# Performance work log

Measured on AMD Instinct MI355X. Metric: run time of the kernel, lower is better.

Reference implementation:

```python
import jax, jax.numpy as jnp
import numpy as np

L, DM, H, DK, DV, DFF = 4, 1024, 16, 64, 64, 4096
B, T, S = 4, 1024, 1024
EPS = 1e-5


def layer_norm(x):
    m = jnp.mean(x, axis=-1, keepdims=True)
    v = jnp.mean((x - m) ** 2, axis=-1, keepdims=True)
    return (x - m) / jnp.sqrt(v + EPS)


def mha(x_q, x_kv, Wq, Wk, Wv, Wo, mask):
    # x_q: [B,Lq,DM], x_kv: [B,Lk,DM], W*: [DM, H*DK] (pre-transposed), Wo: [H*DV, DM]
    b, lq, _ = x_q.shape
    lk = x_kv.shape[1]
    Q = (x_q @ Wq).reshape(b, lq, H, DK).transpose(0, 2, 1, 3)   # [B,H,Lq,DK]
    K = (x_kv @ Wk).reshape(b, lk, H, DK).transpose(0, 2, 1, 3)
    V = (x_kv @ Wv).reshape(b, lk, H, DV).transpose(0, 2, 1, 3)
    scores = jnp.einsum('bhqd,bhkd->bhqk', Q, K) / np.sqrt(DK).astype(np.float32)
    scores = jnp.where(mask[:, None, :, :], jnp.float32(-1e9), scores)  # masked_fill_
    attn = jax.nn.softmax(scores, axis=-1)
    ctx = jnp.einsum('bhqk,bhkv->bqhv', attn, V).reshape(b, lq, H * DV)
    out = ctx @ Wo
    return layer_norm(out + x_q)


def ffn(x, W1, W2):
    return layer_norm(jax.nn.relu(x @ W1) @ W2 + x)


def setup_inputs() -> dict:
    key = jax.random.key(0)
    ks = jax.random.split(key, 12)
    sc = 0.02
    inp = {
        'dec_inputs': jax.random.normal(ks[0], (B, T, DM), jnp.float32),
        'enc_outputs': jax.random.normal(ks[1], (B, S, DM), jnp.float32),
        # causal mask per get_attn_subsequence_mask (True = masked)
        'dec_self_attn_mask': jnp.broadcast_to(jnp.triu(jnp.ones((T, T), bool), k=1), (B, T, T)),
        'dec_enc_attn_mask': jnp.zeros((B, T, S), bool),
        'self_Wq': sc * jax.random.normal(ks[2], (L, DM, H * DK), jnp.float32),
        'self_Wk': sc * jax.random.normal(ks[3], (L, DM, H * DK), jnp.float32),
        'self_Wv': sc * jax.random.normal(ks[4], (L, DM, H * DV), jnp.float32),
        'self_Wo': sc * jax.random.normal(ks[5], (L, H * DV, DM), jnp.float32),
        'cross_Wq': sc * jax.random.normal(ks[6], (L, DM, H * DK), jnp.float32),
        'cross_Wk': sc * jax.random.normal(ks[7], (L, DM, H * DK), jnp.float32),
        'cross_Wv': sc * jax.random.normal(ks[8], (L, DM, H * DV), jnp.float32),
        'cross_Wo': sc * jax.random.normal(ks[9], (L, H * DV, DM), jnp.float32),
        'ffn_W1': sc * jax.random.normal(ks[10], (L, DM, DFF), jnp.float32),
        'ffn_W2': sc * jax.random.normal(ks[11], (L, DFF, DM), jnp.float32),
    }
    return inp


def reference(dec_inputs, enc_outputs, dec_self_attn_mask, dec_enc_attn_mask,
              self_Wq, self_Wk, self_Wv, self_Wo,
              cross_Wq, cross_Wk, cross_Wv, cross_Wo,
              ffn_W1, ffn_W2):
    x = dec_inputs
    for l in range(L):  # fixed small layer count
        x = mha(x, x, self_Wq[l], self_Wk[l], self_Wv[l], self_Wo[l], dec_self_attn_mask)
        x = mha(x, enc_outputs, cross_Wq[l], cross_Wk[l], cross_Wv[l], cross_Wo[l], dec_enc_attn_mask)
        x = ffn(x, ffn_W1[l], ffn_W2[l])
    return x
```

## Files before the change

kernel.cpp:

```cpp
#include <hip/hip_runtime.h>

typedef unsigned short u16;
typedef unsigned int u32;
typedef __bf16 bf16x8 __attribute__((ext_vector_type(8)));
typedef float f32x4 __attribute__((ext_vector_type(4)));

#define TT 1024

__device__ __forceinline__ u16 f2bf(float f) {
  u32 u = __float_as_uint(f);
  u32 r = (u + 0x7fffu + ((u >> 16) & 1u)) >> 16;
  return (u16)r;
}
__device__ __forceinline__ float bf2f(u16 b) {
  return __uint_as_float(((u32)b) << 16);
}

__device__ __forceinline__ void gl_lds16(const void* g, void* l) {
  __builtin_amdgcn_global_load_lds(
      (const __attribute__((address_space(1))) u32*)g,
      (__attribute__((address_space(3))) u32*)l, 16, 0, 0);
}

__global__ __launch_bounds__(256) void k_f32_to_bf16(const float* __restrict__ in,
                                                     u16* __restrict__ out, int n) {
  int i = (blockIdx.x * 256 + threadIdx.x) * 4;
  if (i >= n) return;
  float4 v = *(const float4*)(in + i);
  ushort4 o;
  o.x = f2bf(v.x); o.y = f2bf(v.y); o.z = f2bf(v.z); o.w = f2bf(v.w);
  *(ushort4*)(out + i) = o;
}

__global__ __launch_bounds__(256) void k_init(const float* __restrict__ in,
                                              u16* __restrict__ bfo,
                                              float* __restrict__ fo, int n) {
  int i = (blockIdx.x * 256 + threadIdx.x) * 4;
  if (i >= n) return;
  float4 v = *(const float4*)(in + i);
  ushort4 o;
  o.x = f2bf(v.x); o.y = f2bf(v.y); o.z = f2bf(v.z); o.w = f2bf(v.w);
  *(ushort4*)(bfo + i) = o;
  *(float4*)(fo + i) = v;
}

struct TPack {
  const float* src[8];
  u16* dst[8];
};
__global__ __launch_bounds__(256) void k_transpose(TPack p, int R, int C) {
  __shared__ float tile[32][33];
  const int tx = threadIdx.x & 31;
  const int ty = threadIdx.x >> 5;
  const float* __restrict__ src = p.src[blockIdx.z];
  u16* __restrict__ dst = p.dst[blockIdx.z];
  const int c0 = blockIdx.x * 32;
  const int r0 = blockIdx.y * 32;
#pragma unroll
  for (int i = 0; i < 4; i++)
    tile[ty + i * 8][tx] = src[(size_t)(r0 + ty + i * 8) * C + c0 + tx];
  __syncthreads();
#pragma unroll
  for (int i = 0; i < 4; i++)
    dst[(size_t)(c0 + ty + i * 8) * R + r0 + tx] = f2bf(tile[tx][ty + i * 8]);
}

__global__ __launch_bounds__(256) void k_tbf(const u16* __restrict__ src, int ld,
                                             u16* __restrict__ dst) {
  __shared__ u16 tile[32][33];
  const int r0 = blockIdx.y * 32;
  const int c0 = blockIdx.x * 32;
  const int tr = threadIdx.x >> 3;
  const int tc = (threadIdx.x & 7) * 4;
  ushort4 v = *(const ushort4*)&src[(size_t)(r0 + tr) * ld + c0 + tc];
  tile[tr][tc] = v.x; tile[tr][tc + 1] = v.y; tile[tr][tc + 2] = v.z; tile[tr][tc + 3] = v.w;
  __syncthreads();
  ushort4 o;
  o.x = tile[tc][tr]; o.y = tile[tc + 1][tr]; o.z = tile[tc + 2][tr]; o.w = tile[tc + 3][tr];
  *(ushort4*)&dst[(size_t)(c0 + tr) * 4096 + r0 + tc] = o;
}

template <int OUT_BF16, int RELU, int SPLITK>
__global__ __launch_bounds__(256) void k_gemm_tn(const u16* __restrict__ A,
                                                 const u16* __restrict__ Bt,
                                                 void* __restrict__ Cout,
                                                 void* __restrict__ Cout2,
                                                 int M, int N, int K) {
  __shared__ __attribute__((aligned(16))) u16 sA[128 * 32];
  __shared__ __attribute__((aligned(16))) u16 sB[128 * 32];
  const int tid = threadIdx.x;
  const int wave = tid >> 6;
  const int lane = tid & 63;
  const int quad = lane >> 4;
  const int lc = lane & 15;
  const int m0 = blockIdx.x * 128;
  const int n0 = blockIdx.y * 128;
  const int wr = (wave >> 1) * 64;
  const int wc = (wave & 1) * 64;

  const int Ks = K / SPLITK;
  const size_t kOff = (size_t)blockIdx.z * Ks;

  const int c0 = wave * 2, c1 = wave * 2 + 1;
  const int srow = lane >> 2;
  const int scol = (lane & 3) * 8;

  const u16* a0 = A + (size_t)(m0 + c0 * 16 + srow) * K + kOff + scol;
  const u16* a1 = A + (size_t)(m0 + c1 * 16 + srow) * K + kOff + scol;
  const u16* b0 = Bt + (size_t)(n0 + c0 * 16 + srow) * K + kOff + scol;
  const u16* b1 = Bt + (size_t)(n0 + c1 * 16 + srow) * K + kOff + scol;
  u16* lA0 = sA + c0 * 512;
  u16* lA1 = sA + c1 * 512;
  u16* lB0 = sB + c0 * 512;
  u16* lB1 = sB + c1 * 512;

  f32x4 acc[4][4];
  const f32x4 z4 = {0.f, 0.f, 0.f, 0.f};
#pragma unroll
  for (int i = 0; i < 4; i++)
#pragma unroll
    for (int j = 0; j < 4; j++) acc[i][j] = z4;

  for (int k0 = 0; k0 < Ks; k0 += 32) {
    __syncthreads();
    gl_lds16(a0, lA0);
    gl_lds16(a1, lA1);
    gl_lds16(b0, lB0);
    gl_lds16(b1, lB1);
    a0 += 32; a1 += 32; b0 += 32; b1 += 32;
    __syncthreads();
    bf16x8 af[4], bfr[4];
#pragma unroll
    for (int i = 0; i < 4; i++)
      af[i] = *(const bf16x8*)&sA[(wr + i * 16 + lc) * 32 + quad * 8];
#pragma unroll
    for (int j = 0; j < 4; j++)
      bfr[j] = *(const bf16x8*)&sB[(wc + j * 16 + lc) * 32 + quad * 8];
#pragma unroll
    for (int i = 0; i < 4; i++)
#pragma unroll
      for (int j = 0; j < 4; j++)
        acc[i][j] = __builtin_amdgcn_mfma_f32_16x16x32_bf16(af[i], bfr[j], acc[i][j], 0, 0, 0);
  }

  void* Cw = (SPLITK > 1 && blockIdx.z == 1) ? Cout2 : Cout;
#pragma unroll
  for (int i = 0; i < 4; i++) {
    const int row = m0 + wr + i * 16 + quad * 4;
#pragma unroll
    for (int j = 0; j < 4; j++) {
      const int col = n0 + wc + j * 16 + lc;
#pragma unroll
      for (int r = 0; r < 4; r++) {
        float v = acc[i][j][r];
        if (RELU) v = fmaxf(v, 0.f);
        if (OUT_BF16)
          ((u16*)Cw)[(size_t)(row + r) * N + col] = f2bf(v);
        else
          ((float*)Cw)[(size_t)(row + r) * N + col] = v;
      }
    }
  }
}

template <int CAUSAL>
__global__ __launch_bounds__(256, 4) void k_flash(const u16* __restrict__ Q, int ldq,
                                                  const u16* __restrict__ K, int ldk,
                                                  const u16* __restrict__ Vt,
                                                  u16* __restrict__ O) {
  __shared__ __attribute__((aligned(16))) u16 sK[2][64 * 64];
  __shared__ __attribute__((aligned(16))) u16 sV[2][64 * 64];
  __shared__ __attribute__((aligned(16))) u16 sP[4][16 * 64];
  const int tid = threadIdx.x;
  const int wave = tid >> 6;
  const int lane = tid & 63;
  const int quad = lane >> 4;
  const int lc = lane & 15;
  const int qb = blockIdx.x;
  const int b = blockIdx.y >> 4;
  const int h = blockIdx.y & 15;
  const size_t rowB = (size_t)b * TT;
  const int qrow = qb * 64 + wave * 16;
  const int hc = h * 64;

  const bf16x8 qf0 = *(const bf16x8*)&Q[(rowB + qrow + lc) * ldq + hc + quad * 8];
  const bf16x8 qf1 = *(const bf16x8*)&Q[(rowB + qrow + lc) * ldq + hc + 32 + quad * 8];

  f32x4 o[4];
  float m_r[4], l_r[4];
  const f32x4 z4 = {0.f, 0.f, 0.f, 0.f};
#pragma unroll
  for (int d = 0; d < 4; d++) o[d] = z4;
#pragma unroll
  for (int r = 0; r < 4; r++) { m_r[r] = -1e30f; l_r[r] = 0.f; }

  const float cvt = 1.4426950408889634f / 8.0f;
  u16* myP = sP[wave];
  const int l7 = lc & 7;
  const int swr = (lc >> 2) | ((lc & 1) << 2);
  const int p_lo = wave * 64 + lane;

  const int nkt = CAUSAL ? (qb + 1) : 16;

  auto stage = [&](int cur, int s0) {
#pragma unroll
    for (int half = 0; half < 2; half++) {
      const int p = half * 256 + p_lo;
      const int row = p >> 3;
      const int cb = (p & 7) ^ (row & 7);
      const int p0 = half * 256 + wave * 64;
      gl_lds16(K + (rowB + s0 + row) * (size_t)ldk + hc + cb * 8, &sK[cur][p0 * 8]);
      gl_lds16(Vt + (size_t)(hc + row) * 4096 + rowB + s0 + cb * 8, &sV[cur][p0 * 8]);
    }
  };

  stage(0, 0);
  int cur = 0;
  for (int kt = 0; kt < nkt; kt++) {
    const int s0 = kt * 64;
    __syncthreads();
    if (kt + 1 < nkt) stage(cur ^ 1, s0 + 64);

    f32x4 s[4];
#pragma unroll
    for (int st = 0; st < 4; st++) {
      const int key = st * 16 + lc;
      const bf16x8 kf0 = *(const bf16x8*)&sK[cur][key * 64 + ((quad ^ l7) * 8)];
      const bf16x8 kf1 = *(const bf16x8*)&sK[cur][key * 64 + (((4 + quad) ^ l7) * 8)];
      f32x4 z = z4;
      z = __builtin_amdgcn_mfma_f32_16x16x32_bf16(qf0, kf0, z, 0, 0, 0);
      z = __builtin_amdgcn_mfma_f32_16x16x32_bf16(qf1, kf1, z, 0, 0, 0);
      s[st] = z;
    }

#pragma unroll
    for (int r = 0; r < 4; r++) {
      float sv0 = s[0][r] * cvt, sv1 = s[1][r] * cvt;
      float sv2 = s[2][r] * cvt, sv3 = s[3][r] * cvt;
      if (CAUSAL) {
        const int qg = qrow + quad * 4 + r;
        if (s0 + lc > qg) sv0 = -1e30f;
        if (s0 + 16 + lc > qg) sv1 = -1e30f;
        if (s0 + 32 + lc > qg) sv2 = -1e30f;
        if (s0 + 48 + lc > qg) sv3 = -1e30f;
      }
      float pm = fmaxf(fmaxf(sv0, sv1), fmaxf(sv2, sv3));
      pm = fmaxf(pm, __shfl_xor(pm, 1));
      pm = fmaxf(pm, __shfl_xor(pm, 2));
      pm = fmaxf(pm, __shfl_xor(pm, 4));
      pm = fmaxf(pm, __shfl_xor(pm, 8));
      const float mn = fmaxf(m_r[r], pm);
      const float al = exp2f(m_r[r] - mn);
      m_r[r] = mn;
      const float p0 = exp2f(sv0 - mn);
      const float p1 = exp2f(sv1 - mn);
      const float p2 = exp2f(sv2 - mn);
      const float p3 = exp2f(sv3 - mn);
      l_r[r] = l_r[r] * al + (p0 + p1 + p2 + p3);
      const int row = quad * 4 + r;
      const int sw = quad | ((r & 1) << 2);
      u16* pr = myP + row * 64 + l7;
      pr[(((lc >> 3) | 0) ^ sw) * 8] = f2bf(p0);
      pr[(((lc >> 3) | 2) ^ sw) * 8] = f2bf(p1);
      pr[(((lc >> 3) | 4) ^ sw) * 8] = f2bf(p2);
      pr[(((lc >> 3) | 6) ^ sw) * 8] = f2bf(p3);
#pragma unroll
      for (int d = 0; d < 4; d++) o[d][r] *= al;
    }

#pragma unroll
    for (int c = 0; c < 2; c++) {
      const bf16x8 pf = *(const bf16x8*)&myP[lc * 64 + (((c * 4 + quad) ^ swr) * 8)];
#pragma unroll
      for (int d = 0; d < 4; d++) {
        const int dv = d * 16 + lc;
        const bf16x8 vf = *(const bf16x8*)&sV[cur][dv * 64 + (((c * 4 + quad) ^ l7) * 8)];
        o[d] = __builtin_amdgcn_mfma_f32_16x16x32_bf16(pf, vf, o[d], 0, 0, 0);
      }
    }
    cur ^= 1;
  }

#pragma unroll
  for (int r = 0; r < 4; r++) {
    float l = l_r[r];
    l += __shfl_xor(l, 1);
    l += __shfl_xor(l, 2);
    l += __shfl_xor(l, 4);
    l += __shfl_xor(l, 8);
    const float inv = 1.0f / l;
    const size_t orow = (rowB + qrow + quad * 4 + r) * 1024 + hc;
#pragma unroll
    for (int d = 0; d < 4; d++) O[orow + d * 16 + lc] = f2bf(o[d][r] * inv);
  }
}

template <int NSUM>
__global__ __launch_bounds__(256) void k_ln(const float* __restrict__ y0,
                                            const float* __restrict__ y1,
                                            float* __restrict__ xf,
                                            u16* __restrict__ xb,
                                            float* __restrict__ fout) {
  const int row = blockIdx.x;
  const int tid = threadIdx.x;
  const int lane = tid & 63, wave = tid >> 6;
  const size_t base = (size_t)row * 1024 + tid * 4;
  float4 v = *(const float4*)&y0[base];
  float4 xv = *(const float4*)&xf[base];
  if (NSUM == 2) {
    float4 w = *(const float4*)&y1[base];
    v.x += w.x; v.y += w.y; v.z += w.z; v.w += w.w;
  }
  v.x += xv.x; v.y += xv.y; v.z += xv.z; v.w += xv.w;
  float s = v.x + v.y + v.z + v.w;
  float ss = v.x * v.x + v.y * v.y + v.z * v.z + v.w * v.w;
#pragma unroll
  for (int off = 1; off < 64; off <<= 1) {
    s += __shfl_xor(s, off);
    ss += __shfl_xor(ss, off);
  }
  __shared__ float rs[4], rss[4];
  if (lane == 0) { rs[wave] = s; rss[wave] = ss; }
  __syncthreads();
  const float S = rs[0] + rs[1] + rs[2] + rs[3];
  const float SS = rss[0] + rss[1] + rss[2] + rss[3];
  const float mean = S * (1.f / 1024.f);
  const float var = SS * (1.f / 1024.f) - mean * mean;
  const float inv = rsqrtf(var + 1e-5f);
  const float o0 = (v.x - mean) * inv, o1 = (v.y - mean) * inv;
  const float o2 = (v.z - mean) * inv, o3 = (v.w - mean) * inv;
  float4 fo; fo.x = o0; fo.y = o1; fo.z = o2; fo.w = o3;
  *(float4*)&xf[base] = fo;
  ushort4 ob;
  ob.x = f2bf(o0); ob.y = f2bf(o1); ob.z = f2bf(o2); ob.w = f2bf(o3);
  *(ushort4*)&xb[base] = ob;
  if (fout) *(float4*)&fout[base] = fo;
}

extern "C" void kernel_launch(void* const* d_in, const int* in_sizes, int n_in,
                              void* d_out, int out_size, void* d_ws, size_t ws_size,
                              hipStream_t stream) {
  const float* dec_inputs  = (const float*)d_in[0];
  const float* enc_outputs = (const float*)d_in[1];
  const float* self_Wq = (const float*)d_in[4];
  const float* self_Wk = (const float*)d_in[5];
  const float* self_Wv = (const float*)d_in[6];
  const float* self_Wo = (const float*)d_in[7];
  const float* cross_Wq = (const float*)d_in[8];
  const float* cross_Wk = (const float*)d_in[9];
  const float* cross_Wv = (const float*)d_in[10];
  const float* cross_Wo = (const float*)d_in[11];
  const float* ffn_W1 = (const float*)d_in[12];
  const float* ffn_W2 = (const float*)d_in[13];

  char* ws = (char*)d_ws;
  const size_t MB = 1024 * 1024;
  u16* wq_t = (u16*)(ws + 0 * MB);
  u16* wk_t = (u16*)(ws + 2 * MB);
  u16* wv_t = (u16*)(ws + 4 * MB);
  u16* wo_t = (u16*)(ws + 6 * MB);
  u16* cq_t = (u16*)(ws + 8 * MB);
  u16* ck_t = (u16*)(ws + 10 * MB);
  u16* cv_t = (u16*)(ws + 12 * MB);
  u16* co_t = (u16*)(ws + 14 * MB);
  u16* w1_t = (u16*)(ws + 16 * MB);
  u16* w2_t = (u16*)(ws + 24 * MB);
  u16* encb = (u16*)(ws + 32 * MB);
  u16* xb   = (u16*)(ws + 40 * MB);
  u16* qkv  = (u16*)(ws + 48 * MB);
  u16* kvb  = (u16*)(ws + 56 * MB);
  u16* ctx  = (u16*)(ws + 72 * MB);
  u16* hbuf = (u16*)(ws + 48 * MB);
  float* yb = (float*)(ws + 80 * MB);
  u16* vtb  = (u16*)(ws + 80 * MB);
  float* xf = (float*)(ws + 96 * MB);
  float* ysA = (float*)(ws + 48 * MB);
  float* ysW = (float*)(ws + 0 * MB);

  const int NTOK = 4 * TT * 1024;

  k_init<<<4096, 256, 0, stream>>>(dec_inputs, xb, xf, NTOK);
  k_f32_to_bf16<<<4096, 256, 0, stream>>>(enc_outputs, encb, NTOK);

  for (int l = 0; l < 4; l++) {
    const size_t sqOff = (size_t)l * 1024 * 1024;
    const size_t ffOff = (size_t)l * 4096 * 1024;
    TPack sq;
    sq.src[0] = self_Wq + sqOff;  sq.dst[0] = wq_t;
    sq.src[1] = self_Wk + sqOff;  sq.dst[1] = wk_t;
    sq.src[2] = self_Wv + sqOff;  sq.dst[2] = wv_t;
    sq.src[3] = self_Wo + sqOff;  sq.dst[3] = wo_t;
    sq.src[4] = cross_Wq + sqOff; sq.dst[4] = cq_t;
    sq.src[5] = cross_Wk + sqOff; sq.dst[5] = ck_t;
    sq.src[6] = cross_Wv + sqOff; sq.dst[6] = cv_t;
    sq.src[7] = cross_Wo + sqOff; sq.dst[7] = co_t;
    k_transpose<<<dim3(32, 32, 8), 256, 0, stream>>>(sq, 1024, 1024);
    TPack p1 = sq; p1.src[0] = ffn_W1 + ffOff; p1.dst[0] = w1_t;
    k_transpose<<<dim3(128, 32, 1), 256, 0, stream>>>(p1, 1024, 4096);
    TPack p2 = sq; p2.src[0] = ffn_W2 + ffOff; p2.dst[0] = w2_t;
    k_transpose<<<dim3(32, 128, 1), 256, 0, stream>>>(p2, 4096, 1024);

    k_gemm_tn<1, 0, 1><<<dim3(32, 24), 256, 0, stream>>>(xb, wq_t, qkv, nullptr, 4096, 3072, 1024);
    k_tbf<<<dim3(32, 128), 256, 0, stream>>>(qkv + 2048, 3072, vtb);
    k_flash<1><<<dim3(16, 64), 256, 0, stream>>>(qkv, 3072, qkv + 1024, 3072, vtb, ctx);
    k_gemm_tn<0, 0, 2><<<dim3(32, 8, 2), 256, 0, stream>>>(ctx, wo_t, yb, ysA, 4096, 1024, 1024);
    k_ln<2><<<4096, 256, 0, stream>>>(yb, ysA, xf, xb, nullptr);

    k_gemm_tn<1, 0, 1><<<dim3(32, 8), 256, 0, stream>>>(xb, cq_t, qkv, nullptr, 4096, 1024, 1024);
    k_gemm_tn<1, 0, 1><<<dim3(32, 16), 256, 0, stream>>>(encb, ck_t, kvb, nullptr, 4096, 2048, 1024);
    k_tbf<<<dim3(32, 128), 256, 0, stream>>>(kvb + 1024, 2048, vtb);
    k_flash<0><<<dim3(16, 64), 256, 0, stream>>>(qkv, 1024, kvb, 2048, vtb, ctx);
    k_gemm_tn<0, 0, 2><<<dim3(32, 8, 2), 256, 0, stream>>>(ctx, co_t, yb, ysA, 4096, 1024, 1024);
    k_ln<2><<<4096, 256, 0, stream>>>(yb, ysA, xf, xb, nullptr);

    k_gemm_tn<1, 1, 1><<<dim3(32, 32), 256, 0, stream>>>(xb, w1_t, hbuf, nullptr, 4096, 4096, 1024);
    k_gemm_tn<0, 0, 2><<<dim3(32, 8, 2), 256, 0, stream>>>(hbuf, w2_t, yb, ysW, 4096, 1024, 4096);
    k_ln<2><<<4096, 256, 0, stream>>>(yb, ysW, xf, xb, (l == 3) ? (float*)d_out : nullptr);
  }
}
```

Measured before the change: 1.941 ms.

## Double-buffer GEMM LDS tiles and XOR-swizzle K chunks to avoid bank conflicts

The bf16 MFMA GEMM now keeps two LDS buffers per operand. The next K-tile is prefetched with global_load_lds while the current tile is consumed, which drops one barrier per iteration. It also applies an XOR swizzle to the 8-element K chunk position, on both the global-to-LDS write side and the fragment read side, to reduce LDS bank conflicts. LDS use doubles, which may lower occupancy. Overlap depends on how the compiler places vmcnt waits around the async LDS loads.

```diff
diff --git a/kernel.cpp b/kernel.cpp
--- a/kernel.cpp
+++ b/kernel.cpp
@@ -86,8 +86,8 @@
                                                  void* __restrict__ Cout,
                                                  void* __restrict__ Cout2,
                                                  int M, int N, int K) {
-  __shared__ __attribute__((aligned(16))) u16 sA[128 * 32];
-  __shared__ __attribute__((aligned(16))) u16 sB[128 * 32];
+  __shared__ __attribute__((aligned(16))) u16 sA[2][128 * 32];
+  __shared__ __attribute__((aligned(16))) u16 sB[2][128 * 32];
   const int tid = threadIdx.x;
   const int wave = tid >> 6;
   const int lane = tid & 63;
@@ -103,16 +103,12 @@
 
   const int c0 = wave * 2, c1 = wave * 2 + 1;
   const int srow = lane >> 2;
-  const int scol = (lane & 3) * 8;
+  const int scol = ((lane & 3) ^ ((srow >> 1) & 3)) * 8;
 
   const u16* a0 = A + (size_t)(m0 + c0 * 16 + srow) * K + kOff + scol;
   const u16* a1 = A + (size_t)(m0 + c1 * 16 + srow) * K + kOff + scol;
   const u16* b0 = Bt + (size_t)(n0 + c0 * 16 + srow) * K + kOff + scol;
   const u16* b1 = Bt + (size_t)(n0 + c1 * 16 + srow) * K + kOff + scol;
-  u16* lA0 = sA + c0 * 512;
-  u16* lA1 = sA + c1 * 512;
-  u16* lB0 = sB + c0 * 512;
-  u16* lB1 = sB + c1 * 512;
 
   f32x4 acc[4][4];
   const f32x4 z4 = {0.f, 0.f, 0.f, 0.f};
@@ -121,26 +117,34 @@
 #pragma unroll
     for (int j = 0; j < 4; j++) acc[i][j] = z4;
 
+  const int qs = quad ^ ((lc >> 1) & 3);
+
+  auto stage = [&](int buf) {
+    gl_lds16(a0, &sA[buf][c0 * 512]);
+    gl_lds16(a1, &sA[buf][c1 * 512]);
+    gl_lds16(b0, &sB[buf][c0 * 512]);
+    gl_lds16(b1, &sB[buf][c1 * 512]);
+    a0 += 32; a1 += 32; b0 += 32; b1 += 32;
+  };
+
+  stage(0);
+  int cur = 0;
   for (int k0 = 0; k0 < Ks; k0 += 32) {
     __syncthreads();
-    gl_lds16(a0, lA0);
-    gl_lds16(a1, lA1);
-    gl_lds16(b0, lB0);
-    gl_lds16(b1, lB1);
-    a0 += 32; a1 += 32; b0 += 32; b1 += 32;
-    __syncthreads();
+    if (k0 + 32 < Ks) stage(cur ^ 1);
     bf16x8 af[4], bfr[4];
 #pragma unroll
     for (int i = 0; i < 4; i++)
-      af[i] = *(const bf16x8*)&sA[(wr + i * 16 + lc) * 32 + quad * 8];
+      af[i] = *(const bf16x8*)&sA[cur][(wr + i * 16 + lc) * 32 + qs * 8];
 #pragma unroll
     for (int j = 0; j < 4; j++)
-      bfr[j] = *(const bf16x8*)&sB[(wc + j * 16 + lc) * 32 + quad * 8];
+      bfr[j] = *(const bf16x8*)&sB[cur][(wc + j * 16 + lc) * 32 + qs * 8];
 #pragma unroll
     for (int i = 0; i < 4; i++)
 #pragma unroll
       for (int j = 0; j < 4; j++)
         acc[i][j] = __builtin_amdgcn_mfma_f32_16x16x32_bf16(af[i], bfr[j], acc[i][j], 0, 0, 0);
+    cur ^= 1;
   }
 
   void* Cw = (SPLITK > 1 && blockIdx.z == 1) ? Cout2 : Cout;
```

Result: faster. 1.865 ms (-3.9%).
